# Performance work log

Hardware: AMD Instinct MI355X
Metric: run time of the kernel (lower is better)

Reference implementation:

```python
import jax, jax.numpy as jnp
import numpy as np

LEAKY_SLOPE = 0.2  # tf.nn.leaky_relu default alpha
L2_EPS = 1e-12     # tf.nn.l2_normalize default epsilon


def setup_inputs() -> dict:
    key = jax.random.key(0)
    N, d, E, k = 100000, 64, 1600000, 3
    k0, k1, k2, k3 = jax.random.split(key, 4)
    x = jax.random.normal(k0, (N, d), dtype=jnp.float32)
    edge_index = jax.random.randint(k1, (2, E), 0, N, dtype=jnp.int32)
    scale = 1.0 / np.sqrt(d).astype(np.float32)
    W_gcn = jax.random.normal(k2, (k, d, d), dtype=jnp.float32) * scale
    W_int = jax.random.normal(k3, (k, d, d), dtype=jnp.float32) * scale
    b_gcn = jnp.zeros((k, d), dtype=jnp.float32)
    b_int = jnp.zeros((k, d), dtype=jnp.float32)
    return {"x": x, "edge_index": edge_index, "W_gcn": W_gcn, "b_gcn": b_gcn,
            "W_int": W_int, "b_int": b_int}


def _l2norm(h):
    sq = jnp.sum(h * h, axis=-1, keepdims=True)
    return h * jax.lax.rsqrt(jnp.maximum(sq, L2_EPS))


def reference(x, edge_index, W_gcn, b_gcn, W_int, b_int):
    N = x.shape[0]
    row, col = edge_index[0], edge_index[1]
    # LightGCN.norm_adj: symmetric normalization D^-1/2 A D^-1/2 (no self-loops)
    deg = jax.ops.segment_sum(jnp.ones_like(row, dtype=x.dtype), row, num_segments=N)
    dinv = jnp.where(deg > 0, jax.lax.rsqrt(deg), 0.0)
    w = dinv[row] * dinv[col]  # [E]

    def agg(h):
        # sparse normed_adj @ h : gather source feats, scale, scatter-add to dst
        return jax.ops.segment_sum(w[:, None] * h[col], row, num_segments=N)

    lrelu = lambda z: jax.nn.leaky_relu(z, LEAKY_SLOPE)
    h = x
    outs = [x]
    for i in range(W_gcn.shape[0]):
        ha = agg(h)  # [N, d]
        h = lrelu(ha @ W_gcn[i] + b_gcn[i]) + lrelu((h * ha) @ W_int[i] + b_int[i])
        outs.append(_l2norm(h))
    return jnp.concatenate(outs, axis=-1)  # [N, (k+1)*d]
```

## Files before the change

kernel.cpp:

```cpp
#include <hip/hip_runtime.h>


#define LEAKY 0.2f
#define NBK_MAX 512
#define TILE_A 4096
#define BCAP 5120

typedef unsigned short ushort_t;
typedef short short8 __attribute__((ext_vector_type(8)));
typedef float f32x4 __attribute__((ext_vector_type(4)));

__device__ __forceinline__ float lrelu(float z) { return z > 0.f ? z : LEAKY * z; }

__device__ __forceinline__ unsigned f2bf(float f) {
  unsigned u = __float_as_uint(f);
  return (u + 0x7FFFu + ((u >> 16) & 1u)) >> 16;
}

__device__ __forceinline__ float bf2f(unsigned u) {
  return __uint_as_float(u << 16);
}

__global__ __launch_bounds__(256) void zerotails_k(int* __restrict__ tails, int nbk) {
  int t = blockIdx.x * 256 + threadIdx.x;
  if (t < nbk) tails[t] = 0;
}

__global__ __launch_bounds__(256) void bucket_k(const int* __restrict__ row,
                                                const int* __restrict__ col,
                                                int* __restrict__ tails,
                                                unsigned int* __restrict__ buckets,
                                                int E, int nbk) {
  __shared__ int bcnt[NBK_MAX], bex[NBK_MAX], bnext[NBK_MAX], gbase[NBK_MAX];
  __shared__ int ssc[256];
  int t = threadIdx.x;
  int ts = blockIdx.x * TILE_A;
  int tn = E - ts;
  if (tn > TILE_A) tn = TILE_A;
  bcnt[t] = 0;
  bcnt[t + 256] = 0;
  __syncthreads();
  for (int i = t; i < tn; i += 256) atomicAdd(&bcnt[row[ts + i] >> 8], 1);
  __syncthreads();
  int a0 = bcnt[2 * t], a1 = bcnt[2 * t + 1];
  ssc[t] = a0 + a1;
  __syncthreads();
  #pragma unroll
  for (int off = 1; off < 256; off <<= 1) {
    int x = (t >= off) ? ssc[t - off] : 0;
    __syncthreads();
    ssc[t] += x;
    __syncthreads();
  }
  int ex = ssc[t] - (a0 + a1);
  bex[2 * t] = ex;
  bex[2 * t + 1] = ex + a0;
  bnext[2 * t] = ex;
  bnext[2 * t + 1] = ex + a0;
  if (t < nbk && bcnt[t] > 0) gbase[t] = atomicAdd(&tails[t], bcnt[t]);
  int t2 = t + 256;
  if (t2 < nbk && bcnt[t2] > 0) gbase[t2] = atomicAdd(&tails[t2], bcnt[t2]);
  __syncthreads();
  for (int i = t; i < tn; i += 256) {
    int r = row[ts + i], c = col[ts + i];
    int b = r >> 8;
    int k = atomicAdd(&bnext[b], 1) - bex[b];
    int pos = gbase[b] + k;
    if (pos < BCAP)
      buckets[(size_t)b * BCAP + pos] = ((unsigned)(r & 255) << 24) | (unsigned)c;
  }
}

__global__ __launch_bounds__(512) void bkscan_k(const int* __restrict__ tails,
                                                int* __restrict__ bkbase,
                                                int* __restrict__ rp,
                                                int nbk, int N, int E) {
  __shared__ int s[512];
  int t = threadIdx.x;
  int v = (t < nbk) ? tails[t] : 0;
  s[t] = v;
  __syncthreads();
  #pragma unroll
  for (int off = 1; off < 512; off <<= 1) {
    int x = (t >= off) ? s[t - off] : 0;
    __syncthreads();
    s[t] += x;
    __syncthreads();
  }
  if (t < nbk) bkbase[t] = s[t] - v;
  if (t == 0) rp[N] = E;
}

__global__ __launch_bounds__(256) void csr_k(const int* __restrict__ tails,
                                             const int* __restrict__ bkbase,
                                             const unsigned int* __restrict__ buckets,
                                             int* __restrict__ rp,
                                             float* __restrict__ dinv,
                                             int* __restrict__ packed, int N) {
  __shared__ int cnt[256], sc[256], cnt2[256];
  int b = blockIdx.x, t = threadIdx.x;
  int row0 = b << 8;
  int nrows = N - row0;
  if (nrows > 256) nrows = 256;
  int cb = tails[b];
  if (cb > BCAP) cb = BCAP;
  int base = bkbase[b];
  const unsigned int* ent = buckets + (size_t)b * BCAP;
  cnt[t] = 0;
  __syncthreads();
  for (int i = t; i < cb; i += 256) atomicAdd(&cnt[ent[i] >> 24], 1);
  __syncthreads();
  int v = cnt[t];
  sc[t] = v;
  __syncthreads();
  #pragma unroll
  for (int off = 1; off < 256; off <<= 1) {
    int x = (t >= off) ? sc[t - off] : 0;
    __syncthreads();
    sc[t] += x;
    __syncthreads();
  }
  int ex = sc[t] - v;
  if (t < nrows) {
    rp[row0 + t] = base + ex;
    dinv[row0 + t] = (v > 0) ? rsqrtf((float)v) : 0.f;
  }
  cnt[t] = ex;
  cnt2[t] = 0;
  __syncthreads();
  for (int i = t; i < cb; i += 256) {
    unsigned e = ent[i];
    int rl = e >> 24;
    int slot = atomicAdd(&cnt2[rl], 1);
    packed[base + cnt[rl] + slot] = (int)(e & 0xFFFFFFu);
  }
}

__global__ __launch_bounds__(256) void copyx_k(const float* __restrict__ x,
                                               float* __restrict__ out,
                                               ushort_t* __restrict__ xb,
                                               int N, int ostride4) {
  int total = N * 16;
  int stride = gridDim.x * blockDim.x;
  for (int i = blockIdx.x * blockDim.x + threadIdx.x; i < total; i += stride) {
    int n = i >> 4, c4 = i & 15;
    float4 v = ((const float4*)x)[i];
    ((float4*)out)[(size_t)n * ostride4 + c4] = v;
    unsigned p0 = f2bf(v.x) | (f2bf(v.y) << 16);
    unsigned p1 = f2bf(v.z) | (f2bf(v.w) << 16);
    ((uint2*)xb)[i] = make_uint2(p0, p1);
  }
}

__global__ __launch_bounds__(256) void packw_k(const float* __restrict__ Wg,
                                               const float* __restrict__ Wi,
                                               ushort_t* __restrict__ Wfrag,
                                               int total) {
  int tid = blockIdx.x * 256 + threadIdx.x;
  if (tid >= total) return;
  int lane = tid & 63;
  int kh = (tid >> 6) & 1;
  int nt = (tid >> 7) & 3;
  int gm = (tid >> 9) & 1;
  int ly = tid >> 10;
  const float* W = (gm ? Wi : Wg) + (size_t)ly * 4096;
  int kb = (kh << 5) + ((lane >> 4) << 3);
  int n = (nt << 4) + (lane & 15);
  unsigned u[4];
  #pragma unroll
  for (int j = 0; j < 4; ++j) {
    unsigned lo = f2bf(W[(kb + 2 * j) * 64 + n]);
    unsigned hi = f2bf(W[(kb + 2 * j + 1) * 64 + n]);
    u[j] = lo | (hi << 16);
  }
  ((uint4*)Wfrag)[tid] = make_uint4(u[0], u[1], u[2], u[3]);
}

__global__ __launch_bounds__(256) void agg_k(const int* __restrict__ rp,
                                             const int* __restrict__ packed,
                                             const float* __restrict__ dinv,
                                             const ushort_t* __restrict__ hin,
                                             ushort_t* __restrict__ ha, int N) {
  int wv = (blockIdx.x << 2) + (threadIdx.x >> 6);
  if (wv >= N) return;
  int lane = threadIdx.x & 63;
  int grp = lane >> 3;
  int l8 = lane & 7;
  int s = __builtin_amdgcn_readfirstlane(rp[wv]);
  int e = __builtin_amdgcn_readfirstlane(rp[wv + 1]);
  float dr = __int_as_float(__builtin_amdgcn_readfirstlane(__float_as_int(dinv[wv])));
  float a[8];
  #pragma unroll
  for (int i = 0; i < 8; ++i) a[i] = 0.f;
  int bidx0 = grp << 2;
  for (int ch = s; ch < e; ch += 64) {
    int m = e - ch;
    if (m > 64) m = 64;
    int cl = (lane < m) ? packed[ch + lane] : 0;
    float wl = (lane < m) ? dinv[cl] * dr : 0.f;
    int nit = (m + 7) >> 3;
    #pragma unroll 4
    for (int j = 0; j < nit; ++j) {
      int bi = bidx0 + (j << 5);
      int c = __builtin_amdgcn_ds_bpermute(bi, cl);
      float w = __int_as_float(
          __builtin_amdgcn_ds_bpermute(bi, __float_as_int(wl)));
      uint4 v = ((const uint4*)(hin + ((size_t)c << 6)))[l8];
      a[0] = fmaf(w, __uint_as_float(v.x << 16), a[0]);
      a[1] = fmaf(w, __uint_as_float(v.x & 0xFFFF0000u), a[1]);
      a[2] = fmaf(w, __uint_as_float(v.y << 16), a[2]);
      a[3] = fmaf(w, __uint_as_float(v.y & 0xFFFF0000u), a[3]);
      a[4] = fmaf(w, __uint_as_float(v.z << 16), a[4]);
      a[5] = fmaf(w, __uint_as_float(v.z & 0xFFFF0000u), a[5]);
      a[6] = fmaf(w, __uint_as_float(v.w << 16), a[6]);
      a[7] = fmaf(w, __uint_as_float(v.w & 0xFFFF0000u), a[7]);
    }
  }
  #pragma unroll
  for (int off = 8; off < 64; off <<= 1)
    #pragma unroll
    for (int i = 0; i < 8; ++i) a[i] += __shfl_xor(a[i], off);
  if (grp == 0) {
    unsigned p0 = f2bf(a[0]) | (f2bf(a[1]) << 16);
    unsigned p1 = f2bf(a[2]) | (f2bf(a[3]) << 16);
    unsigned p2 = f2bf(a[4]) | (f2bf(a[5]) << 16);
    unsigned p3 = f2bf(a[6]) | (f2bf(a[7]) << 16);
    ((uint4*)(ha + ((size_t)wv << 6)))[l8] = make_uint4(p0, p1, p2, p3);
  }
}

__global__ __launch_bounds__(256) void gemmM_k(const ushort_t* __restrict__ ha,
                                               const ushort_t* __restrict__ hin,
                                               const ushort_t* __restrict__ Wfrag,
                                               const float* __restrict__ bg,
                                               const float* __restrict__ bi,
                                               ushort_t* __restrict__ hout,
                                               float* __restrict__ outp,
                                               int N, int ntiles, int ostride) {
  int lane = threadIdx.x & 63;
  int gq = lane >> 4, ln15 = lane & 15;
  const short8* wf = (const short8*)Wfrag;
  short8 bG[8], bI[8];
  #pragma unroll
  for (int nt = 0; nt < 4; ++nt)
    #pragma unroll
    for (int kh = 0; kh < 2; ++kh) {
      bG[nt * 2 + kh] = wf[nt * 128 + kh * 64 + lane];
      bI[nt * 2 + kh] = wf[512 + nt * 128 + kh * 64 + lane];
    }
  float bgv[4], biv[4];
  #pragma unroll
  for (int nt = 0; nt < 4; ++nt) {
    bgv[nt] = bg[nt * 16 + ln15];
    biv[nt] = bi[nt * 16 + ln15];
  }
  int wid = (blockIdx.x << 2) + (threadIdx.x >> 6);
  int nw = gridDim.x << 2;
  for (int tile = wid; tile < ntiles; tile += nw) {
    int node0 = tile << 4;
    const short8* pa =
        (const short8*)(ha + (size_t)(node0 + ln15) * 64 + gq * 8);
    const short8* ph =
        (const short8*)(hin + (size_t)(node0 + ln15) * 64 + gq * 8);
    f32x4 acc1[4], acc2[4];
    #pragma unroll
    for (int nt = 0; nt < 4; ++nt) {
      acc1[nt] = (f32x4){bgv[nt], bgv[nt], bgv[nt], bgv[nt]};
      acc2[nt] = (f32x4){biv[nt], biv[nt], biv[nt], biv[nt]};
    }
    #pragma unroll
    for (int kh = 0; kh < 2; ++kh) {
      short8 af = pa[kh * 4];
      short8 hf = ph[kh * 4];
      short8 vmf;
      #pragma unroll
      for (int e2 = 0; e2 < 8; ++e2) {
        float fa = bf2f((ushort_t)af[e2]);
        float fh = bf2f((ushort_t)hf[e2]);
        vmf[e2] = (short)f2bf(fa * fh);
      }
      #pragma unroll
      for (int nt = 0; nt < 4; ++nt) {
        acc1[nt] = __builtin_amdgcn_mfma_f32_16x16x32_bf16(af, bG[nt * 2 + kh],
                                                           acc1[nt], 0, 0, 0);
        acc2[nt] = __builtin_amdgcn_mfma_f32_16x16x32_bf16(vmf, bI[nt * 2 + kh],
                                                           acc2[nt], 0, 0, 0);
      }
    }
    float z[4][4];
    float ssr[4] = {0.f, 0.f, 0.f, 0.f};
    #pragma unroll
    for (int nt = 0; nt < 4; ++nt)
      #pragma unroll
      for (int reg = 0; reg < 4; ++reg) {
        float zz = lrelu(acc1[nt][reg]) + lrelu(acc2[nt][reg]);
        z[nt][reg] = zz;
        ssr[reg] = fmaf(zz, zz, ssr[reg]);
      }
    #pragma unroll
    for (int off = 1; off < 16; off <<= 1)
      #pragma unroll
      for (int reg = 0; reg < 4; ++reg) ssr[reg] += __shfl_xor(ssr[reg], off);
    float inv[4];
    #pragma unroll
    for (int reg = 0; reg < 4; ++reg)
      inv[reg] = rsqrtf(fmaxf(ssr[reg], 1e-12f));
    #pragma unroll
    for (int reg = 0; reg < 4; ++reg) {
      int r = node0 + 4 * gq + reg;
      if (r < N) {
        #pragma unroll
        for (int nt = 0; nt < 4; ++nt) {
          outp[(size_t)r * ostride + nt * 16 + ln15] = z[nt][reg] * inv[reg];
          hout[(size_t)r * 64 + nt * 16 + ln15] = (ushort_t)f2bf(z[nt][reg]);
        }
      }
    }
  }
}

extern "C" void kernel_launch(void* const* d_in, const int* in_sizes, int n_in,
                              void* d_out, int out_size, void* d_ws, size_t ws_size,
                              hipStream_t stream) {
  const float* x  = (const float*)d_in[0];
  const int*   ei = (const int*)d_in[1];
  const float* Wg = (const float*)d_in[2];
  const float* bg = (const float*)d_in[3];
  const float* Wi = (const float*)d_in[4];
  const float* bi = (const float*)d_in[5];
  float* out = (float*)d_out;

  const int d = 64;
  const int N = in_sizes[0] / d;
  const int E = in_sizes[1] / 2;
  const int K = in_sizes[2] / (d * d);
  const int* row = ei;
  const int* col = ei + E;
  const int nbk = (N + 255) / 256;
  const int N16 = (N + 15) & ~15;
  const int ntiles = N16 / 16;
  const int ostride = (K + 1) * d;

  char* ws = (char*)d_ws;
  size_t off = 0;
  auto alloc = [&](size_t bytes) {
    char* p = ws + off;
    off = (off + bytes + 255) & ~(size_t)255;
    return p;
  };
  int*   tails  = (int*)alloc((size_t)NBK_MAX * 4);
  int*   bkbase = (int*)alloc((size_t)NBK_MAX * 4);
  int*   rp     = (int*)alloc((size_t)(N + 1) * 4);
  float* dinv   = (float*)alloc((size_t)N * 4);
  unsigned int* buckets = (unsigned int*)alloc((size_t)nbk * BCAP * 4);
  int*   packed = (int*)alloc((size_t)E * 4);
  ushort_t* ha  = (ushort_t*)alloc((size_t)N16 * d * 2);
  ushort_t* hb0 = (ushort_t*)alloc((size_t)N16 * d * 2);
  ushort_t* hb1 = (ushort_t*)alloc((size_t)N16 * d * 2);
  ushort_t* xb  = (ushort_t*)alloc((size_t)N16 * d * 2);
  ushort_t* Wfrag = (ushort_t*)alloc((size_t)K * 8192 * 2);
  (void)ws_size;

  zerotails_k<<<(nbk + 255) / 256, 256, 0, stream>>>(tails, nbk);
  int ntA = (E + TILE_A - 1) / TILE_A;
  bucket_k<<<ntA, 256, 0, stream>>>(row, col, tails, buckets, E, nbk);
  bkscan_k<<<1, 512, 0, stream>>>(tails, bkbase, rp, nbk, N, E);
  csr_k<<<nbk, 256, 0, stream>>>(tails, bkbase, buckets, rp, dinv, packed, N);
  copyx_k<<<2048, 256, 0, stream>>>(x, out, xb, N, ostride / 4);
  int wtotal = K * 1024;
  packw_k<<<(wtotal + 255) / 256, 256, 0, stream>>>(Wg, Wi, Wfrag, wtotal);

  const ushort_t* hin = xb;
  ushort_t* bufs[2] = {hb0, hb1};
  for (int i = 0; i < K; ++i) {
    ushort_t* hout = bufs[i & 1];
    agg_k<<<(N + 3) / 4, 256, 0, stream>>>(rp, packed, dinv, hin, ha, N);
    gemmM_k<<<1024, 256, 0, stream>>>(
        ha, hin, Wfrag + (size_t)i * 8192, bg + (size_t)i * d,
        bi + (size_t)i * d, hout, out + (size_t)(i + 1) * d, N, ntiles, ostride);
    hin = hout;
  }
}
```

Before: 234.9 us.

## Prescale features by source dinv to drop per-edge weight gather in aggregation

The symmetric normalization is factored so each node's features are stored a second time, pre-multiplied by its dinv (from copyx and from the GEMM epilogue). Aggregation then sums the prescaled neighbour rows with a mask and multiplies by the destination dinv once at the end. This removes the random per-edge dinv[col] gather and one bpermute per edge. In exchange, every layer writes an extra bf16 feature array, and rounding the scaled values to bf16 slightly changes numerics.

```diff
diff --git a/kernel.cpp b/kernel.cpp
--- a/kernel.cpp
+++ b/kernel.cpp
@@ -137,8 +137,10 @@
 }
 
 __global__ __launch_bounds__(256) void copyx_k(const float* __restrict__ x,
+                                               const float* __restrict__ dinv,
                                                float* __restrict__ out,
                                                ushort_t* __restrict__ xb,
+                                               ushort_t* __restrict__ xg,
                                                int N, int ostride4) {
   int total = N * 16;
   int stride = gridDim.x * blockDim.x;
@@ -149,6 +151,10 @@
     unsigned p0 = f2bf(v.x) | (f2bf(v.y) << 16);
     unsigned p1 = f2bf(v.z) | (f2bf(v.w) << 16);
     ((uint2*)xb)[i] = make_uint2(p0, p1);
+    float dv = dinv[n];
+    unsigned q0 = f2bf(v.x * dv) | (f2bf(v.y * dv) << 16);
+    unsigned q1 = f2bf(v.z * dv) | (f2bf(v.w * dv) << 16);
+    ((uint2*)xg)[i] = make_uint2(q0, q1);
   }
 }
 
@@ -179,7 +185,7 @@
 __global__ __launch_bounds__(256) void agg_k(const int* __restrict__ rp,
                                              const int* __restrict__ packed,
                                              const float* __restrict__ dinv,
-                                             const ushort_t* __restrict__ hin,
+                                             const ushort_t* __restrict__ gin,
                                              ushort_t* __restrict__ ha, int N) {
   int wv = (blockIdx.x << 2) + (threadIdx.x >> 6);
   if (wv >= N) return;
@@ -197,23 +203,20 @@
     int m = e - ch;
     if (m > 64) m = 64;
     int cl = (lane < m) ? packed[ch + lane] : 0;
-    float wl = (lane < m) ? dinv[cl] * dr : 0.f;
     int nit = (m + 7) >> 3;
     #pragma unroll 4
     for (int j = 0; j < nit; ++j) {
-      int bi = bidx0 + (j << 5);
-      int c = __builtin_amdgcn_ds_bpermute(bi, cl);
-      float w = __int_as_float(
-          __builtin_amdgcn_ds_bpermute(bi, __float_as_int(wl)));
-      uint4 v = ((const uint4*)(hin + ((size_t)c << 6)))[l8];
-      a[0] = fmaf(w, __uint_as_float(v.x << 16), a[0]);
-      a[1] = fmaf(w, __uint_as_float(v.x & 0xFFFF0000u), a[1]);
-      a[2] = fmaf(w, __uint_as_float(v.y << 16), a[2]);
-      a[3] = fmaf(w, __uint_as_float(v.y & 0xFFFF0000u), a[3]);
-      a[4] = fmaf(w, __uint_as_float(v.z << 16), a[4]);
-      a[5] = fmaf(w, __uint_as_float(v.z & 0xFFFF0000u), a[5]);
-      a[6] = fmaf(w, __uint_as_float(v.w << 16), a[6]);
-      a[7] = fmaf(w, __uint_as_float(v.w & 0xFFFF0000u), a[7]);
+      int c = __builtin_amdgcn_ds_bpermute(bidx0 + (j << 5), cl);
+      float msk = ((j << 3) + grp < m) ? 1.f : 0.f;
+      uint4 v = ((const uint4*)(gin + ((size_t)c << 6)))[l8];
+      a[0] = fmaf(msk, __uint_as_float(v.x << 16), a[0]);
+      a[1] = fmaf(msk, __uint_as_float(v.x & 0xFFFF0000u), a[1]);
+      a[2] = fmaf(msk, __uint_as_float(v.y << 16), a[2]);
+      a[3] = fmaf(msk, __uint_as_float(v.y & 0xFFFF0000u), a[3]);
+      a[4] = fmaf(msk, __uint_as_float(v.z << 16), a[4]);
+      a[5] = fmaf(msk, __uint_as_float(v.z & 0xFFFF0000u), a[5]);
+      a[6] = fmaf(msk, __uint_as_float(v.w << 16), a[6]);
+      a[7] = fmaf(msk, __uint_as_float(v.w & 0xFFFF0000u), a[7]);
     }
   }
   #pragma unroll
@@ -221,10 +224,10 @@
     #pragma unroll
     for (int i = 0; i < 8; ++i) a[i] += __shfl_xor(a[i], off);
   if (grp == 0) {
-    unsigned p0 = f2bf(a[0]) | (f2bf(a[1]) << 16);
-    unsigned p1 = f2bf(a[2]) | (f2bf(a[3]) << 16);
-    unsigned p2 = f2bf(a[4]) | (f2bf(a[5]) << 16);
-    unsigned p3 = f2bf(a[6]) | (f2bf(a[7]) << 16);
+    unsigned p0 = f2bf(a[0] * dr) | (f2bf(a[1] * dr) << 16);
+    unsigned p1 = f2bf(a[2] * dr) | (f2bf(a[3] * dr) << 16);
+    unsigned p2 = f2bf(a[4] * dr) | (f2bf(a[5] * dr) << 16);
+    unsigned p3 = f2bf(a[6] * dr) | (f2bf(a[7] * dr) << 16);
     ((uint4*)(ha + ((size_t)wv << 6)))[l8] = make_uint4(p0, p1, p2, p3);
   }
 }
@@ -234,7 +237,9 @@
                                                const ushort_t* __restrict__ Wfrag,
                                                const float* __restrict__ bg,
                                                const float* __restrict__ bi,
+                                               const float* __restrict__ dinv,
                                                ushort_t* __restrict__ hout,
+                                               ushort_t* __restrict__ gout,
                                                float* __restrict__ outp,
                                                int N, int ntiles, int ostride) {
   int lane = threadIdx.x & 63;
@@ -309,10 +314,13 @@
     for (int reg = 0; reg < 4; ++reg) {
       int r = node0 + 4 * gq + reg;
       if (r < N) {
+        float dv = dinv[r];
         #pragma unroll
         for (int nt = 0; nt < 4; ++nt) {
           outp[(size_t)r * ostride + nt * 16 + ln15] = z[nt][reg] * inv[reg];
           hout[(size_t)r * 64 + nt * 16 + ln15] = (ushort_t)f2bf(z[nt][reg]);
+          gout[(size_t)r * 64 + nt * 16 + ln15] =
+              (ushort_t)f2bf(z[nt][reg] * dv);
         }
       }
     }
@@ -358,6 +366,9 @@
   ushort_t* hb0 = (ushort_t*)alloc((size_t)N16 * d * 2);
   ushort_t* hb1 = (ushort_t*)alloc((size_t)N16 * d * 2);
   ushort_t* xb  = (ushort_t*)alloc((size_t)N16 * d * 2);
+  ushort_t* hg0 = (ushort_t*)alloc((size_t)N16 * d * 2);
+  ushort_t* hg1 = (ushort_t*)alloc((size_t)N16 * d * 2);
+  ushort_t* xg  = (ushort_t*)alloc((size_t)N16 * d * 2);
   ushort_t* Wfrag = (ushort_t*)alloc((size_t)K * 8192 * 2);
   (void)ws_size;
 
@@ -366,18 +377,23 @@
   bucket_k<<<ntA, 256, 0, stream>>>(row, col, tails, buckets, E, nbk);
   bkscan_k<<<1, 512, 0, stream>>>(tails, bkbase, rp, nbk, N, E);
   csr_k<<<nbk, 256, 0, stream>>>(tails, bkbase, buckets, rp, dinv, packed, N);
-  copyx_k<<<2048, 256, 0, stream>>>(x, out, xb, N, ostride / 4);
+  copyx_k<<<2048, 256, 0, stream>>>(x, dinv, out, xb, xg, N, ostride / 4);
   int wtotal = K * 1024;
   packw_k<<<(wtotal + 255) / 256, 256, 0, stream>>>(Wg, Wi, Wfrag, wtotal);
 
   const ushort_t* hin = xb;
-  ushort_t* bufs[2] = {hb0, hb1};
+  const ushort_t* gin = xg;
+  ushort_t* hbufs[2] = {hb0, hb1};
+  ushort_t* gbufs[2] = {hg0, hg1};
   for (int i = 0; i < K; ++i) {
-    ushort_t* hout = bufs[i & 1];
-    agg_k<<<(N + 3) / 4, 256, 0, stream>>>(rp, packed, dinv, hin, ha, N);
+    ushort_t* hout = hbufs[i & 1];
+    ushort_t* gout = gbufs[i & 1];
+    agg_k<<<(N + 3) / 4, 256, 0, stream>>>(rp, packed, dinv, gin, ha, N);
     gemmM_k<<<1024, 256, 0, stream>>>(
         ha, hin, Wfrag + (size_t)i * 8192, bg + (size_t)i * d,
-        bi + (size_t)i * d, hout, out + (size_t)(i + 1) * d, N, ntiles, ostride);
+        bi + (size_t)i * d, dinv, hout, gout, out + (size_t)(i + 1) * d,
+        N, ntiles, ostride);
     hin = hout;
-  }
-}
+    gin = gout;
+  }
+}
```

Measured after the change: 234.1 us. No clear change (-0.4%).
